# Kernel tuning notes

Hardware: AMD Instinct MI355X
Metric: run time of the kernel (lower is better)

## Reference

```python
import jax, jax.numpy as jnp
import numpy as np

N_HEAD = 8
D_MODEL = 512
D_HEAD = D_MODEL // N_HEAD
D_HIDDEN = 2048
LN_EPS = 1e-5


def setup_inputs() -> dict:
    key = jax.random.key(0)
    ks = jax.random.split(key, 13)
    s = 0.02
    return {
        "spatial_features": jax.random.normal(ks[0], (4096, 64, D_MODEL), dtype=jnp.float32),
        "Wk": jax.random.normal(ks[1], (D_MODEL, D_MODEL), dtype=jnp.float32) * s,
        "bk": jnp.zeros((D_MODEL,), dtype=jnp.float32),
        "Wv": jax.random.normal(ks[2], (D_MODEL, D_MODEL), dtype=jnp.float32) * s,
        "bv": jnp.zeros((D_MODEL,), dtype=jnp.float32),
        "score_w": jax.random.normal(ks[3], (N_HEAD, D_HEAD), dtype=jnp.float32) * s,
        "score_b": jnp.zeros((N_HEAD,), dtype=jnp.float32),
        "W1": jax.random.normal(ks[4], (D_MODEL, D_HIDDEN), dtype=jnp.float32) * s,
        "b1": jnp.zeros((D_HIDDEN,), dtype=jnp.float32),
        "W2": jax.random.normal(ks[5], (D_HIDDEN, D_MODEL), dtype=jnp.float32) * s,
        "b2": jnp.zeros((D_MODEL,), dtype=jnp.float32),
        "ln_g": jnp.ones((D_MODEL,), dtype=jnp.float32),
        "ln_b": jnp.zeros((D_MODEL,), dtype=jnp.float32),
    }


def reference(spatial_features, Wk, bk, Wv, bv, score_w, score_b,
              W1, b1, W2, b2, ln_g, ln_b):
    B, N, _ = spatial_features.shape
    # k, v projections -> [B, N, H, Dh]
    k = (spatial_features @ Wk + bk).reshape(B, N, N_HEAD, D_HEAD)
    v = (spatial_features @ Wv + bv).reshape(B, N, N_HEAD, D_HEAD)
    # per-head score: Linear(d_head -> 1) batched over heads
    score = jnp.einsum('bnhd,hd->bnh', k, score_w) + score_b  # [B, N, H]
    attn = jax.nn.softmax(score, axis=1)                       # softmax over N
    # weighted sum pooling over N, then concat heads -> [B, d_model]
    feature = jnp.einsum('bnh,bnhd->bhd', attn, v).reshape(B, D_MODEL)
    # FFN with residual + layernorm (dropout = eval identity)
    h = jax.nn.gelu(feature @ W1 + b1, approximate=False)
    y = h @ W2 + b2 + feature
    mu = jnp.mean(y, axis=-1, keepdims=True)
    var = jnp.mean((y - mu) ** 2, axis=-1, keepdims=True)
    out = (y - mu) * jax.lax.rsqrt(var + LN_EPS) * ln_g + ln_b
    return out
```

## Files before the change

### kernel.cpp

```cpp
#include <hip/hip_runtime.h>
#include <hip/hip_bf16.h>

#define N_HEAD 8
#define D_MODEL 512
#define D_HEAD 64
#define D_HIDDEN 2048
#define NTOK 64
#define BATCH 4096

typedef __attribute__((ext_vector_type(4))) float f32x4;
typedef __attribute__((ext_vector_type(8))) short short8;
typedef __attribute__((ext_vector_type(8))) unsigned short u16x8;
typedef __attribute__((ext_vector_type(4))) unsigned short u16x4;

__device__ __forceinline__ float bf2f(unsigned short u) {
    return __uint_as_float(((unsigned int)u) << 16);
}
__device__ __forceinline__ unsigned short f2bf(float f) {
    unsigned int b = __float_as_uint(f);
    b += 0x7fffu + ((b >> 16) & 1u);
    return (unsigned short)(b >> 16);
}
__device__ __forceinline__ float wave_sum(float v) {
    v += __shfl_xor(v, 32); v += __shfl_xor(v, 16); v += __shfl_xor(v, 8);
    v += __shfl_xor(v, 4);  v += __shfl_xor(v, 2);  v += __shfl_xor(v, 1);
    return v;
}
__device__ __forceinline__ void gload_lds16(const void* g, void* l) {
    __builtin_amdgcn_global_load_lds(
        (const __attribute__((address_space(1))) unsigned int*)g,
        (__attribute__((address_space(3))) unsigned int*)l, 16, 0, 0);
}

__global__ __launch_bounds__(256) void prep_all(
    const float* __restrict__ Wk, const float* __restrict__ score_w,
    const float* __restrict__ Wv, const float* __restrict__ W1,
    const float* __restrict__ W2,
    unsigned short* __restrict__ uT,
    unsigned short* __restrict__ WvT, unsigned short* __restrict__ W1T,
    unsigned short* __restrict__ W2T) {
    int m = blockIdx.y;
    if (m == 3) {
        int idx = blockIdx.x * 256 + threadIdx.x;
        if (idx < 16 * 512) {
            int h = idx & 15, c = idx >> 4;
            float s = 0.f;
            if (h < 8) {
                #pragma unroll 8
                for (int d = 0; d < D_HEAD; ++d)
                    s += Wk[c * D_MODEL + h * D_HEAD + d] * score_w[h * D_HEAD + d];
            }
            uT[h * D_MODEL + c] = f2bf(s);
        }
        return;
    }
    const float* in; unsigned short* out; int K, N, tX, tiles;
    if (m == 0)      { in = Wv; out = WvT; K = 512;  N = 512;  tX = 16; tiles = 256;  }
    else if (m == 1) { in = W1; out = W1T; K = 512;  N = 2048; tX = 64; tiles = 1024; }
    else             { in = W2; out = W2T; K = 2048; N = 512;  tX = 16; tiles = 1024; }
    int t = blockIdx.x;
    if (t >= tiles) return;
    int n0 = (t % tX) * 32, k0 = (t / tX) * 32;
    __shared__ float tile[32][33];
    int tx = threadIdx.x & 31, ty = threadIdx.x >> 5;
    #pragma unroll
    for (int i = ty; i < 32; i += 8)
        tile[i][tx] = in[(size_t)(k0 + i) * N + n0 + tx];
    __syncthreads();
    #pragma unroll
    for (int i = ty; i < 32; i += 8)
        out[(size_t)(n0 + i) * K + k0 + tx] = f2bf(tile[tx][i]);
}

__global__ void score_pool_v14(
    const float* __restrict__ x, const unsigned short* __restrict__ uT,
    unsigned short* __restrict__ pooled) {
    __shared__ unsigned short xl[16 * D_MODEL];
    __shared__ unsigned short ul[8 * D_MODEL];
    __shared__ float el[16 * 8];
    __shared__ float zacc[8];

    const int tid = threadIdx.x;
    const int l = tid & 63, w = tid >> 6;
    const int hg = l >> 4, lr = l & 15;

    {
        int r = tid >> 6;
        int c8 = (tid & 63) * 8;
        u16x8 v = *(const u16x8*)(uT + r * D_MODEL + c8);
        *(u16x8*)&ul[r * D_MODEL + (c8 ^ (r << 3))] = v;
    }

    const int tr4 = tid >> 7;
    const int col4 = (tid & 127) * 4;

    const int c2 = (tid & 255) * 2;
    const int hh = tid >> 8;

    const int b0 = blockIdx.x * 4;

    float4 pre[4];
    {
        const float4* p = (const float4*)(x + (size_t)b0 * (NTOK * D_MODEL));
        #pragma unroll
        for (int j = 0; j < 4; ++j) pre[j] = p[j * 512 + tid];
    }

    f32x4 acc0 = {0.f, 0.f, 0.f, 0.f};
    f32x4 acc1 = {0.f, 0.f, 0.f, 0.f};

    #pragma unroll 1
    for (int qq = 0; qq < 16; ++qq) {
        const int q = qq & 3;
        if (q == 0 && tid < 8) zacc[tid] = 0.f;
        #pragma unroll
        for (int j = 0; j < 4; ++j) {
            int row = j * 4 + tr4;
            float4 a = pre[j];
            u16x4 ov = {f2bf(a.x), f2bf(a.y), f2bf(a.z), f2bf(a.w)};
            *(u16x4*)&xl[row * D_MODEL + (col4 ^ ((row & 7) << 3))] = ov;
        }
        if (qq < 15) {
            const int nb = b0 + ((qq + 1) >> 2), nq = (qq + 1) & 3;
            const float4* p = (const float4*)(x + (size_t)nb * (NTOK * D_MODEL) +
                                              nq * 16 * D_MODEL);
            #pragma unroll
            for (int j = 0; j < 4; ++j) pre[j] = p[j * 512 + tid];
        }
        asm volatile("s_waitcnt lgkmcnt(0)" ::: "memory");
        __builtin_amdgcn_s_barrier();

        if (w == (qq & 7)) {
            f32x4 sacc = {0.f, 0.f, 0.f, 0.f};
            const int rbase = lr * D_MODEL;
            const int rsw = (lr & 7) << 3;
            #pragma unroll
            for (int ks = 0; ks < 16; ++ks) {
                int off = ks * 32 + hg * 8;
                short8 uf;
                if (lr < 8) uf = *(const short8*)&ul[lr * D_MODEL + (off ^ (lr << 3))];
                else        uf = (short8){0, 0, 0, 0, 0, 0, 0, 0};
                short8 xf = *(const short8*)&xl[rbase + (off ^ rsw)];
                sacc = __builtin_amdgcn_mfma_f32_16x16x32_bf16(uf, xf, sacc, 0, 0, 0);
            }
            f32x4 ev;
            float zsum[4];
            #pragma unroll
            for (int j = 0; j < 4; ++j) {
                float e = __expf(sacc[j]);
                ev[j] = e;
                e += __shfl_xor(e, 1); e += __shfl_xor(e, 2);
                e += __shfl_xor(e, 4); e += __shfl_xor(e, 8);
                zsum[j] = e;
            }
            if (hg < 2) {
                *(f32x4*)&el[lr * 8 + hg * 4] = ev;
                if (lr == 0) {
                    f32x4 z = *(const f32x4*)&zacc[hg * 4];
                    z[0] += zsum[0]; z[1] += zsum[1];
                    z[2] += zsum[2]; z[3] += zsum[3];
                    *(f32x4*)&zacc[hg * 4] = z;
                }
            }
        }
        asm volatile("s_waitcnt lgkmcnt(0)" ::: "memory");
        __builtin_amdgcn_s_barrier();

        #pragma unroll 4
        for (int t = 0; t < 16; ++t) {
            unsigned int xw = *(const unsigned int*)&xl[t * D_MODEL +
                                                        (c2 ^ ((t & 7) << 3))];
            f32x4 e4 = *(const f32x4*)&el[t * 8 + hh * 4];
            float xa = __uint_as_float(xw << 16);
            float xb = __uint_as_float(xw & 0xffff0000u);
            acc0 += e4 * xa;
            acc1 += e4 * xb;
        }
        if (q == 3) {
            f32x4 z = *(const f32x4*)&zacc[hh * 4];
            unsigned short* pb = pooled + (size_t)(b0 + (qq >> 2)) * (N_HEAD * D_MODEL);
            #pragma unroll
            for (int hq = 0; hq < 4; ++hq) {
                float rzq = 1.f / z[hq];
                unsigned int pk = (unsigned int)f2bf(acc0[hq] * rzq) |
                                  ((unsigned int)f2bf(acc1[hq] * rzq) << 16);
                *(unsigned int*)(pb + (hh * 4 + hq) * D_MODEL + c2) = pk;
            }
            acc0 = (f32x4){0.f, 0.f, 0.f, 0.f};
            acc1 = (f32x4){0.f, 0.f, 0.f, 0.f};
        }
        asm volatile("s_waitcnt lgkmcnt(0)" ::: "memory");
        __builtin_amdgcn_s_barrier();
    }
}

template <int BM, int BN, int MODE>
__global__ __launch_bounds__(256) void gemm_mf(
    const unsigned short* __restrict__ A, int lda,
    const unsigned short* __restrict__ BT,
    const float* __restrict__ bias,
    void* __restrict__ Cout, int ldc,
    const unsigned short* __restrict__ res, int K) {
    __shared__ unsigned short Al[BM * 64];
    __shared__ unsigned short Bl[BN * 64];
    int m0 = blockIdx.x * BM;
    int n0;
    const unsigned short* Ap = A;
    const unsigned short* Bp;
    const float* bp;
    if (MODE == 0) {
        int h = blockIdx.y;
        Ap = A + (size_t)h * 512;
        Bp = BT + (size_t)h * 64 * K;
        bp = bias + h * 64;
        n0 = h * 64;
    } else {
        n0 = blockIdx.y * BN;
        Bp = BT + (size_t)n0 * K;
        bp = bias + n0;
    }
    int tid = threadIdx.x, l = tid & 63, w = tid >> 6;
    int lr = l & 15, lq = l >> 4;
    int wm = w >> 1, wn = w & 1;
    constexpr int MR = BM / 32, NR = BN / 32;
    constexpr int AI = BM / 8, BI = BN / 8;

    f32x4 acc[MR][NR];
    #pragma unroll
    for (int mi = 0; mi < MR; ++mi)
        #pragma unroll
        for (int nj = 0; nj < NR; ++nj) acc[mi][nj] = (f32x4){0.f, 0.f, 0.f, 0.f};

    int srow = l >> 3;
    int scol = ((l & 7) ^ ((l >> 3) & 7)) << 3;

    for (int k0 = 0; k0 < K; k0 += 64) {
        #pragma unroll
        for (int j = 0; j < AI / 4; ++j) {
            int ji = w * (AI / 4) + j;
            const unsigned short* src = Ap + (size_t)(m0 + ji * 8 + srow) * lda + k0 + scol;
            gload_lds16(src, &Al[ji * 512]);
        }
        #pragma unroll
        for (int j = 0; j < BI / 4; ++j) {
            int ji = w * (BI / 4) + j;
            const unsigned short* src = Bp + (size_t)(ji * 8 + srow) * K + k0 + scol;
            gload_lds16(src, &Bl[ji * 512]);
        }
        __syncthreads();
        #pragma unroll
        for (int kk = 0; kk < 64; kk += 32) {
            int sw = (kk + lq * 8) ^ ((l & 7) << 3);
            short8 af[MR], bf[NR];
            #pragma unroll
            for (int mi = 0; mi < MR; ++mi)
                af[mi] = *(const short8*)&Al[(wm * (BM / 2) + mi * 16 + lr) * 64 + sw];
            #pragma unroll
            for (int nj = 0; nj < NR; ++nj)
                bf[nj] = *(const short8*)&Bl[(wn * (BN / 2) + nj * 16 + lr) * 64 + sw];
            #pragma unroll
            for (int mi = 0; mi < MR; ++mi)
                #pragma unroll
                for (int nj = 0; nj < NR; ++nj)
                    acc[mi][nj] = __builtin_amdgcn_mfma_f32_16x16x32_bf16(
                        af[mi], bf[nj], acc[mi][nj], 0, 0, 0);
        }
        __syncthreads();
    }

    #pragma unroll
    for (int mi = 0; mi < MR; ++mi) {
        #pragma unroll
        for (int nj = 0; nj < NR; ++nj) {
            #pragma unroll
            for (int j = 0; j < 4; ++j) {
                int row = m0 + wm * (BM / 2) + mi * 16 + lq * 4 + j;
                int nl = wn * (BN / 2) + nj * 16 + lr;
                int col = n0 + nl;
                float v = acc[mi][nj][j] + bp[nl];
                if (MODE == 1) {
                    v = 0.5f * v * (1.0f + erff(v * 0.70710678118654752f));
                }
                if (MODE == 2) {
                    v += bf2f(res[(size_t)row * 512 + col]);
                    ((float*)Cout)[(size_t)row * ldc + col] = v;
                } else {
                    ((unsigned short*)Cout)[(size_t)row * ldc + col] = f2bf(v);
                }
            }
        }
    }
}

__global__ __launch_bounds__(256) void ln_kernel(
    float* __restrict__ y, const float* __restrict__ g, const float* __restrict__ bta) {
    int row = blockIdx.x * 4 + (threadIdx.x >> 6);
    int l = threadIdx.x & 63;
    float* yp = y + (size_t)row * D_MODEL;
    float4 v0 = *(const float4*)(yp + l * 8);
    float4 v1 = *(const float4*)(yp + l * 8 + 4);
    float vv[8] = {v0.x, v0.y, v0.z, v0.w, v1.x, v1.y, v1.z, v1.w};
    float s = 0.f;
    #pragma unroll
    for (int i = 0; i < 8; ++i) s += vv[i];
    s = wave_sum(s);
    float mean = s * (1.f / 512.f);
    float q = 0.f;
    #pragma unroll
    for (int i = 0; i < 8; ++i) { float d = vv[i] - mean; q += d * d; }
    q = wave_sum(q);
    float rstd = rsqrtf(q * (1.f / 512.f) + 1e-5f);
    float4 g0 = *(const float4*)(g + l * 8);
    float4 g1 = *(const float4*)(g + l * 8 + 4);
    float4 b0 = *(const float4*)(bta + l * 8);
    float4 b1 = *(const float4*)(bta + l * 8 + 4);
    float gv[8] = {g0.x, g0.y, g0.z, g0.w, g1.x, g1.y, g1.z, g1.w};
    float bv[8] = {b0.x, b0.y, b0.z, b0.w, b1.x, b1.y, b1.z, b1.w};
    float ov[8];
    #pragma unroll
    for (int i = 0; i < 8; ++i) ov[i] = (vv[i] - mean) * rstd * gv[i] + bv[i];
    float4 o0 = {ov[0], ov[1], ov[2], ov[3]};
    float4 o1 = {ov[4], ov[5], ov[6], ov[7]};
    *(float4*)(yp + l * 8) = o0;
    *(float4*)(yp + l * 8 + 4) = o1;
}

extern "C" void kernel_launch(void* const* d_in, const int* in_sizes, int n_in,
                              void* d_out, int out_size, void* d_ws, size_t ws_size,
                              hipStream_t stream) {
    const float* x       = (const float*)d_in[0];
    const float* Wk      = (const float*)d_in[1];
    const float* Wv      = (const float*)d_in[3];
    const float* bv      = (const float*)d_in[4];
    const float* score_w = (const float*)d_in[5];
    const float* W1      = (const float*)d_in[7];
    const float* b1      = (const float*)d_in[8];
    const float* W2      = (const float*)d_in[9];
    const float* b2      = (const float*)d_in[10];
    const float* ln_g    = (const float*)d_in[11];
    const float* ln_b    = (const float*)d_in[12];
    float* out = (float*)d_out;

    char* ws = (char*)d_ws;
    size_t off = 0;
    auto alloc = [&](size_t sz) {
        void* p = ws + off;
        off = (off + sz + 1023) & ~(size_t)1023;
        return p;
    };
    unsigned short* uT  = (unsigned short*)alloc((size_t)16 * D_MODEL * 2);
    unsigned short* WvT = (unsigned short*)alloc((size_t)512 * 512 * 2);
    unsigned short* W1T = (unsigned short*)alloc((size_t)2048 * 512 * 2);
    unsigned short* W2T = (unsigned short*)alloc((size_t)512 * 2048 * 2);
    unsigned short* pooled = (unsigned short*)alloc((size_t)BATCH * N_HEAD * D_MODEL * 2);
    unsigned short* feat   = (unsigned short*)alloc((size_t)BATCH * D_MODEL * 2);
    unsigned short* Hbuf   = (unsigned short*)alloc((size_t)BATCH * D_HIDDEN * 2);

    prep_all<<<dim3(1024, 4), dim3(256), 0, stream>>>(
        Wk, score_w, Wv, W1, W2, uT, WvT, W1T, W2T);
    score_pool_v14<<<dim3(1024), dim3(512), 0, stream>>>(x, uT, pooled);
    gemm_mf<128, 64, 0><<<dim3(32, 8), dim3(256), 0, stream>>>(
        pooled, N_HEAD * D_MODEL, WvT, bv, (void*)feat, D_MODEL,
        (const unsigned short*)nullptr, 512);
    gemm_mf<128, 128, 1><<<dim3(32, 16), dim3(256), 0, stream>>>(
        feat, D_MODEL, W1T, b1, (void*)Hbuf, D_HIDDEN,
        (const unsigned short*)nullptr, 512);
    gemm_mf<64, 128, 2><<<dim3(64, 4), dim3(256), 0, stream>>>(
        Hbuf, D_HIDDEN, W2T, b2, (void*)out, D_MODEL, feat, 2048);
    ln_kernel<<<dim3(1024), dim3(256), 0, stream>>>(out, ln_g, ln_b);
}
```

Measured before the change: 207.4 us.

## Double-buffer score scratch, drop per-tile barrier, pool directly from global fp32

```diff
diff --git a/kernel.cpp b/kernel.cpp
--- a/kernel.cpp
+++ b/kernel.cpp
@@ -72,13 +72,13 @@
         out[(size_t)(n0 + i) * K + k0 + tx] = f2bf(tile[tx][i]);
 }
 
-__global__ void score_pool_v14(
+__global__ void score_pool_v17(
     const float* __restrict__ x, const unsigned short* __restrict__ uT,
     unsigned short* __restrict__ pooled) {
     __shared__ unsigned short xl[16 * D_MODEL];
     __shared__ unsigned short ul[8 * D_MODEL];
-    __shared__ float el[16 * 8];
-    __shared__ float zacc[8];
+    __shared__ float el[2][16 * 8];
+    __shared__ float zacc[2][8];
 
     const int tid = threadIdx.x;
     const int l = tid & 63, w = tid >> 6;
@@ -94,10 +94,10 @@
     const int tr4 = tid >> 7;
     const int col4 = (tid & 127) * 4;
 
-    const int c2 = (tid & 255) * 2;
+    const int cpair = tid & 255;
     const int hh = tid >> 8;
 
-    const int b0 = blockIdx.x * 4;
+    const int b0 = blockIdx.x * 8;
 
     float4 pre[4];
     {
@@ -110,9 +110,9 @@
     f32x4 acc1 = {0.f, 0.f, 0.f, 0.f};
 
     #pragma unroll 1
-    for (int qq = 0; qq < 16; ++qq) {
+    for (int qq = 0; qq < 32; ++qq) {
         const int q = qq & 3;
-        if (q == 0 && tid < 8) zacc[tid] = 0.f;
+        const int bb = qq >> 2;
         #pragma unroll
         for (int j = 0; j < 4; ++j) {
             int row = j * 4 + tr4;
@@ -120,7 +120,7 @@
             u16x4 ov = {f2bf(a.x), f2bf(a.y), f2bf(a.z), f2bf(a.w)};
             *(u16x4*)&xl[row * D_MODEL + (col4 ^ ((row & 7) << 3))] = ov;
         }
-        if (qq < 15) {
+        if (qq < 31) {
             const int nb = b0 + ((qq + 1) >> 2), nq = (qq + 1) & 3;
             const float4* p = (const float4*)(x + (size_t)nb * (NTOK * D_MODEL) +
                                               nq * 16 * D_MODEL);
@@ -154,43 +154,48 @@
                 zsum[j] = e;
             }
             if (hg < 2) {
-                *(f32x4*)&el[lr * 8 + hg * 4] = ev;
+                *(f32x4*)&el[qq & 1][lr * 8 + hg * 4] = ev;
                 if (lr == 0) {
-                    f32x4 z = *(const f32x4*)&zacc[hg * 4];
-                    z[0] += zsum[0]; z[1] += zsum[1];
-                    z[2] += zsum[2]; z[3] += zsum[3];
-                    *(f32x4*)&zacc[hg * 4] = z;
+                    const int zb = bb & 1;
+                    f32x4 z;
+                    if (q == 0) {
+                        z = (f32x4){zsum[0], zsum[1], zsum[2], zsum[3]};
+                    } else {
+                        z = *(const f32x4*)&zacc[zb][hg * 4];
+                        z[0] += zsum[0]; z[1] += zsum[1];
+                        z[2] += zsum[2]; z[3] += zsum[3];
+                    }
+                    *(f32x4*)&zacc[zb][hg * 4] = z;
                 }
             }
         }
         asm volatile("s_waitcnt lgkmcnt(0)" ::: "memory");
         __builtin_amdgcn_s_barrier();
 
-        #pragma unroll 4
-        for (int t = 0; t < 16; ++t) {
-            unsigned int xw = *(const unsigned int*)&xl[t * D_MODEL +
-                                                        (c2 ^ ((t & 7) << 3))];
-            f32x4 e4 = *(const f32x4*)&el[t * 8 + hh * 4];
-            float xa = __uint_as_float(xw << 16);
-            float xb = __uint_as_float(xw & 0xffff0000u);
-            acc0 += e4 * xa;
-            acc1 += e4 * xb;
+        {
+            const float2* xq = (const float2*)(x + (size_t)(b0 + bb) * (NTOK * D_MODEL) +
+                                               (size_t)q * 16 * D_MODEL) + cpair;
+            #pragma unroll 4
+            for (int tk = 0; tk < 16; ++tk) {
+                float2 xv = xq[tk * 256];
+                f32x4 e4 = *(const f32x4*)&el[qq & 1][tk * 8 + hh * 4];
+                acc0 += e4 * xv.x;
+                acc1 += e4 * xv.y;
+            }
         }
         if (q == 3) {
-            f32x4 z = *(const f32x4*)&zacc[hh * 4];
-            unsigned short* pb = pooled + (size_t)(b0 + (qq >> 2)) * (N_HEAD * D_MODEL);
+            f32x4 z = *(const f32x4*)&zacc[bb & 1][hh * 4];
+            unsigned short* pb = pooled + (size_t)(b0 + bb) * (N_HEAD * D_MODEL);
             #pragma unroll
             for (int hq = 0; hq < 4; ++hq) {
                 float rzq = 1.f / z[hq];
                 unsigned int pk = (unsigned int)f2bf(acc0[hq] * rzq) |
                                   ((unsigned int)f2bf(acc1[hq] * rzq) << 16);
-                *(unsigned int*)(pb + (hh * 4 + hq) * D_MODEL + c2) = pk;
+                *(unsigned int*)(pb + (hh * 4 + hq) * D_MODEL + cpair * 2) = pk;
             }
             acc0 = (f32x4){0.f, 0.f, 0.f, 0.f};
             acc1 = (f32x4){0.f, 0.f, 0.f, 0.f};
         }
-        asm volatile("s_waitcnt lgkmcnt(0)" ::: "memory");
-        __builtin_amdgcn_s_barrier();
     }
 }
 
@@ -358,7 +363,7 @@
 
     prep_all<<<dim3(1024, 4), dim3(256), 0, stream>>>(
         Wk, score_w, Wv, W1, W2, uT, WvT, W1T, W2T);
-    score_pool_v14<<<dim3(1024), dim3(512), 0, stream>>>(x, uT, pooled);
+    score_pool_v17<<<dim3(512), dim3(512), 0, stream>>>(x, uT, pooled);
     gemm_mf<128, 64, 0><<<dim3(32, 8), dim3(256), 0, stream>>>(
         pooled, N_HEAD * D_MODEL, WvT, bv, (void*)feat, D_MODEL,
         (const unsigned short*)nullptr, 512);
```

Measured after the change: 243.5 us. +17.4%, slower.
